# Kernel optimization log

Measured on AMD Instinct MI355X. Metric: run time of the kernel, lower is better.

## Reference

```python
import jax, jax.numpy as jnp
import numpy as np

B, T, E, H = 2, 2048, 1024, 16
S = E // H
LN_EPS = 1e-5


def _layer_norm(x, w, b):
    # normalize over last axis (head dim s)
    mu = jnp.mean(x, axis=-1, keepdims=True)
    var = jnp.mean(jnp.square(x - mu), axis=-1, keepdims=True)
    return (x - mu) * jax.lax.rsqrt(var + LN_EPS) * w + b


def setup_inputs() -> dict:
    key = jax.random.key(0)
    ks = jax.random.split(key, 7)
    scale = 0.02
    return {
        "queries": jax.random.normal(ks[0], (B, T, E), dtype=jnp.float32),
        "keys": jax.random.normal(ks[1], (B, T, E), dtype=jnp.float32),
        "values": jax.random.normal(ks[2], (B, T, E), dtype=jnp.float32),
        "Wq": jax.random.normal(ks[3], (E, E), dtype=jnp.float32) * scale,
        "Wk": jax.random.normal(ks[4], (E, E), dtype=jnp.float32) * scale,
        "Wv": jax.random.normal(ks[5], (E, E), dtype=jnp.float32) * scale,
        "Wo": jax.random.normal(ks[6], (E, E), dtype=jnp.float32) * scale,
        "bo": jnp.zeros((E,), dtype=jnp.float32),
        "q_ln_w": jnp.ones((S,), dtype=jnp.float32),
        "q_ln_b": jnp.zeros((S,), dtype=jnp.float32),
        "k_ln_w": jnp.ones((S,), dtype=jnp.float32),
        "k_ln_b": jnp.zeros((S,), dtype=jnp.float32),
    }


def reference(queries, keys, values, Wq, Wk, Wv, Wo, bo, q_ln_w, q_ln_b, k_ln_w, k_ln_b):
    b, tq, e = queries.shape
    tk = keys.shape[1]
    h, s = H, S

    q = (queries @ Wq).reshape(b, tq, h, s)
    k = (keys @ Wk).reshape(b, tk, h, s)
    v = (values @ Wv).reshape(b, tk, h, s)

    # kqnorm: per-head LayerNorm over s
    q = _layer_norm(q, q_ln_w, q_ln_b)
    k = _layer_norm(k, k_ln_w, k_ln_b)

    # NOTE: original scales q and k each by emb**(-1/4) (NOT head_dim)
    inv4 = jnp.asarray(e, q.dtype) ** -0.25
    q = q * inv4
    k = k * inv4

    dot = jnp.einsum("bqhs,bkhs->bhqk", q, k)  # [b,h,tq,tk]

    # causal mask (mask_diagonal=False -> keep diagonal): mask j > i
    causal = jnp.tril(jnp.ones((tq, tk), dtype=bool))
    dot = jnp.where(causal, dot, jnp.asarray(-jnp.inf, dot.dtype))

    attn = jax.nn.softmax(dot, axis=-1)

    out = jnp.einsum("bhqk,bkhs->bqhs", attn, v).reshape(b, tq, e)
    return out @ Wo + bo
```

## Files before the change

### kernel.cpp

```cpp
#include <hip/hip_runtime.h>

#define Tdim 2048
#define Edim 1024
#define Hdim 16
#define Sdim 64
#define Mdim 4096
#define LN_EPS 1e-5f
#define QKSCALE 0.21233045007200477f

typedef __bf16 bf16x8 __attribute__((ext_vector_type(8)));
typedef float f32x4 __attribute__((ext_vector_type(4)));

__device__ __forceinline__ unsigned short f2bf(float f) {
  union { float f; unsigned int u; } c; c.f = f;
  unsigned int u = c.u;
  return (unsigned short)((u + 0x7FFFu + ((u >> 16) & 1u)) >> 16);
}

__device__ __forceinline__ float exp2fast(float x) {
  float r;
  asm("v_exp_f32 %0, %1" : "=v"(r) : "v"(x));
  return r;
}

__device__ __forceinline__ void gl_lds16(const void* g, void* l) {
  __builtin_amdgcn_global_load_lds(
      (const __attribute__((address_space(1))) void*)g,
      (__attribute__((address_space(3))) void*)l, 16, 0, 0);
}

__device__ __forceinline__ unsigned int pk2bf(unsigned int lo, unsigned int hi) {
  return __builtin_amdgcn_perm(hi, lo, 0x07060302u);
}

__global__ __launch_bounds__(256) void cvt_k(
    const float* __restrict__ X0, const float* __restrict__ X1, const float* __restrict__ X2,
    unsigned short* __restrict__ Y0, unsigned short* __restrict__ Y1,
    unsigned short* __restrict__ Y2) {
  const float* X = blockIdx.z == 0 ? X0 : blockIdx.z == 1 ? X1 : X2;
  unsigned short* Y = blockIdx.z == 0 ? Y0 : blockIdx.z == 1 ? Y1 : Y2;
  size_t i = ((size_t)blockIdx.x * 256 + threadIdx.x) * 8;
  uint4 a = *(const uint4*)&X[i];
  uint4 b = *(const uint4*)&X[i + 4];
  uint4 o;
  o.x = pk2bf(a.x, a.y);
  o.y = pk2bf(a.z, a.w);
  o.z = pk2bf(b.x, b.y);
  o.w = pk2bf(b.z, b.w);
  *(uint4*)&Y[i] = o;
}

__global__ __launch_bounds__(256) void wconv_k(
    const float* __restrict__ W0, const float* __restrict__ W1,
    const float* __restrict__ W2, const float* __restrict__ W3,
    unsigned short* __restrict__ O0, unsigned short* __restrict__ O1,
    unsigned short* __restrict__ O2, unsigned short* __restrict__ O3) {
  const float* W = blockIdx.z == 0 ? W0 : blockIdx.z == 1 ? W1 : blockIdx.z == 2 ? W2 : W3;
  unsigned short* O = blockIdx.z == 0 ? O0 : blockIdx.z == 1 ? O1 : blockIdx.z == 2 ? O2 : O3;
  __shared__ float tile[32][33];
  int n0 = blockIdx.x * 32, k0 = blockIdx.y * 32;
  int tx = threadIdx.x, ty = threadIdx.y;
  for (int yy = ty; yy < 32; yy += 8)
    tile[yy][tx] = W[(size_t)(k0 + yy) * Edim + n0 + tx];
  __syncthreads();
  for (int yy = ty; yy < 32; yy += 8)
    O[(size_t)(n0 + yy) * Edim + k0 + tx] = f2bf(tile[tx][yy]);
}

__global__ __launch_bounds__(256) void qkv_k(
    const unsigned short* __restrict__ Qa, const unsigned short* __restrict__ Ka,
    const unsigned short* __restrict__ Va,
    const unsigned short* __restrict__ Bq, const unsigned short* __restrict__ Bk,
    const unsigned short* __restrict__ Bv,
    const float* __restrict__ qlnw, const float* __restrict__ qlnb,
    const float* __restrict__ klnw, const float* __restrict__ klnb,
    unsigned short* __restrict__ Oq, unsigned short* __restrict__ Ok,
    unsigned short* __restrict__ Ov) {
  __shared__ unsigned short As[2][128 * 64];
  __shared__ unsigned short Bs[2][128 * 64];
  int f = blockIdx.x;
  int L = (f & 7) * 96 + (f >> 3);
  int bx = L & 7, by = (L >> 3) & 31, z = L >> 8;
  const unsigned short* A = z == 0 ? Qa : z == 1 ? Ka : Va;
  const unsigned short* Bt = z == 0 ? Bq : z == 1 ? Bk : Bv;
  const float* lnw = z == 0 ? qlnw : klnw;
  const float* lnb = z == 0 ? qlnb : klnb;
  unsigned short* obf = z == 0 ? Oq : z == 1 ? Ok : Ov;

  int tid = threadIdx.x, lane = tid & 63, w = tid >> 6;
  int wr = w >> 1, wc = w & 1;
  int lg = lane >> 4, l15 = lane & 15;
  int lr = lane >> 3, ls = lane & 7;
  int m0 = by * 128, n0 = bx * 128;

  f32x4 acc[4][4];
#pragma unroll
  for (int i = 0; i < 4; ++i)
#pragma unroll
    for (int j = 0; j < 4; ++j) acc[i][j] = f32x4{0.f, 0.f, 0.f, 0.f};

  auto stage = [&](int buf, int ks) {
    int k0 = ks * 64;
#pragma unroll
    for (int q = 0; q < 4; ++q) {
      int c = w * 4 + q, r = c * 8 + lr;
      gl_lds16(&A[(size_t)(m0 + r) * Edim + k0 + ((ls ^ (r & 7)) * 8)], &As[buf][c * 512]);
    }
#pragma unroll
    for (int q = 0; q < 4; ++q) {
      int c = w * 4 + q, r = c * 8 + lr;
      gl_lds16(&Bt[(size_t)(n0 + r) * Edim + k0 + ((ls ^ (r & 7)) * 8)], &Bs[buf][c * 512]);
    }
  };

  stage(0, 0);
  for (int ks = 0; ks < 16; ++ks) {
    int cur = ks & 1;
    __syncthreads();
    if (ks + 1 < 16) stage(cur ^ 1, ks + 1);
    const unsigned short* pA = (z == 2) ? &Bs[cur][0] : &As[cur][0];
    const unsigned short* pB = (z == 2) ? &As[cur][0] : &Bs[cur][0];
    __builtin_amdgcn_s_setprio(1);
#pragma unroll
    for (int kx = 0; kx < 2; ++kx) {
      bf16x8 a[4], bb[4];
#pragma unroll
      for (int i = 0; i < 4; ++i) {
        int r = wr * 64 + i * 16 + l15;
        a[i] = *(const bf16x8*)&pA[r * 64 + (((kx * 4 + lg) ^ (r & 7)) * 8)];
      }
#pragma unroll
      for (int j = 0; j < 4; ++j) {
        int r = wc * 64 + j * 16 + l15;
        bb[j] = *(const bf16x8*)&pB[r * 64 + (((kx * 4 + lg) ^ (r & 7)) * 8)];
      }
#pragma unroll
      for (int i = 0; i < 4; ++i)
#pragma unroll
        for (int j = 0; j < 4; ++j)
          acc[i][j] = __builtin_amdgcn_mfma_f32_16x16x32_bf16(a[i], bb[j], acc[i][j], 0, 0, 0);
    }
    __builtin_amdgcn_s_setprio(0);
  }

  if (z < 2) {
    int mb = m0 + wr * 64;
    int h = (n0 >> 6) + wc;
#pragma unroll
    for (int i = 0; i < 4; ++i) {
#pragma unroll
      for (int r = 0; r < 4; ++r) {
        float xv[4];
#pragma unroll
        for (int j = 0; j < 4; ++j) xv[j] = acc[i][j][r];
        float sum = xv[0] + xv[1] + xv[2] + xv[3];
        float sq = xv[0] * xv[0] + xv[1] * xv[1] + xv[2] * xv[2] + xv[3] * xv[3];
#pragma unroll
        for (int off = 1; off < 16; off <<= 1) {
          sum += __shfl_xor(sum, off);
          sq += __shfl_xor(sq, off);
        }
        float mean = sum * (1.f / 64.f);
        float var = sq * (1.f / 64.f) - mean * mean;
        float rstd = rsqrtf(var + LN_EPS);
        int m = mb + i * 16 + (lg << 2) + r;
        int bb2 = m >> 11, tt = m & 2047;
        size_t base = ((size_t)(bb2 * Hdim + h) * Tdim + tt) * Sdim;
#pragma unroll
        for (int j = 0; j < 4; ++j) {
          int s = j * 16 + l15;
          float ov = ((xv[j] - mean) * rstd * lnw[s] + lnb[s]) * QKSCALE;
          obf[base + s] = f2bf(ov);
        }
      }
    }
  } else {
#pragma unroll
    for (int i = 0; i < 4; ++i)
#pragma unroll
      for (int r = 0; r < 4; ++r) {
        int hc = n0 + wr * 64 + i * 16 + (lg << 2) + r;
        int h = hc >> 6, s = hc & 63;
#pragma unroll
        for (int j = 0; j < 4; ++j) {
          int tk = m0 + wc * 64 + j * 16 + l15;
          int bb2 = tk >> 11, tt = tk & 2047;
          obf[(((size_t)(bb2 * Hdim + h) * Sdim + s)) * Tdim + tt] = f2bf(acc[i][j][r]);
        }
      }
  }
}

__global__ __launch_bounds__(256) void gemmo_k(
    const unsigned short* __restrict__ A, const unsigned short* __restrict__ Bt,
    const float* __restrict__ bias, float* __restrict__ ofp) {
  __shared__ unsigned short As[2][128 * 64];
  __shared__ unsigned short Bs[2][64 * 64];
  int f = blockIdx.x;
  int L = (f & 7) * 64 + (f >> 3);
  int bx = L & 15, by = L >> 4;
  int tid = threadIdx.x, lane = tid & 63, w = tid >> 6;
  int wr = w >> 1, wc = w & 1;
  int lg = lane >> 4, l15 = lane & 15;
  int lr = lane >> 3, ls = lane & 7;
  int m0 = by * 128, n0 = bx * 64;

  f32x4 acc[4][2];
#pragma unroll
  for (int i = 0; i < 4; ++i)
#pragma unroll
    for (int j = 0; j < 2; ++j) acc[i][j] = f32x4{0.f, 0.f, 0.f, 0.f};

  auto stage = [&](int buf, int ks) {
    int k0 = ks * 64;
#pragma unroll
    for (int q = 0; q < 4; ++q) {
      int c = w * 4 + q, r = c * 8 + lr;
      gl_lds16(&A[(size_t)(m0 + r) * Edim + k0 + ((ls ^ (r & 7)) * 8)], &As[buf][c * 512]);
    }
#pragma unroll
    for (int q = 0; q < 2; ++q) {
      int c = w * 2 + q, r = c * 8 + lr;
      gl_lds16(&Bt[(size_t)(n0 + r) * Edim + k0 + ((ls ^ (r & 7)) * 8)], &Bs[buf][c * 512]);
    }
  };

  stage(0, 0);
  for (int ks = 0; ks < 16; ++ks) {
    int cur = ks & 1;
    __syncthreads();
    if (ks + 1 < 16) stage(cur ^ 1, ks + 1);
    __builtin_amdgcn_s_setprio(1);
#pragma unroll
    for (int kx = 0; kx < 2; ++kx) {
      bf16x8 a[4], bb[2];
#pragma unroll
      for (int i = 0; i < 4; ++i) {
        int r = wr * 64 + i * 16 + l15;
        a[i] = *(const bf16x8*)&As[cur][r * 64 + (((kx * 4 + lg) ^ (r & 7)) * 8)];
      }
#pragma unroll
      for (int j = 0; j < 2; ++j) {
        int r = wc * 32 + j * 16 + l15;
        bb[j] = *(const bf16x8*)&Bs[cur][r * 64 + (((kx * 4 + lg) ^ (r & 7)) * 8)];
      }
#pragma unroll
      for (int i = 0; i < 4; ++i)
#pragma unroll
        for (int j = 0; j < 2; ++j)
          acc[i][j] = __builtin_amdgcn_mfma_f32_16x16x32_bf16(a[i], bb[j], acc[i][j], 0, 0, 0);
    }
    __builtin_amdgcn_s_setprio(0);
  }

  int mb = m0 + wr * 64, nb = n0 + wc * 32;
#pragma unroll
  for (int i = 0; i < 4; ++i)
#pragma unroll
    for (int r = 0; r < 4; ++r) {
      int m = mb + i * 16 + (lg << 2) + r;
#pragma unroll
      for (int j = 0; j < 2; ++j) {
        int n = nb + j * 16 + l15;
        ofp[(size_t)m * Edim + n] = acc[i][j][r] + bias[n];
      }
    }
}

__global__ __launch_bounds__(256) void flash_k(
    const unsigned short* __restrict__ Qn, const unsigned short* __restrict__ Kn,
    const unsigned short* __restrict__ Vb, unsigned short* __restrict__ Ob) {
  __shared__ unsigned short Qs[4096];
  __shared__ unsigned short Ks[2][4096];
  __shared__ unsigned short Vt[2][4096];
  __shared__ unsigned short Ps[4][1024];

  int wid0 = blockIdx.x;
  int idx = wid0 >> 3;
  int bh = (wid0 & 7) * 4 + (idx & 3);
  int qseg = 31 - (idx >> 2);
  int nt = qseg + 1;

  int tid = threadIdx.x, lane = tid & 63, w = tid >> 6;
  int lg = lane >> 4, l15 = lane & 15;
  int lr = lane >> 3, ls = lane & 7;
  const unsigned short* Qg = Qn + ((size_t)bh * Tdim + (size_t)qseg * 64) * Sdim;
  const unsigned short* Kg = Kn + (size_t)bh * Tdim * Sdim;
  const unsigned short* Vg = Vb + (size_t)bh * Sdim * Tdim;
  int b = bh >> 4, h = bh & 15;

  auto stageK = [&](int tt, int kb) {
    const unsigned short* src = Kg + (size_t)tt * 64 * 64;
#pragma unroll
    for (int q = 0; q < 2; ++q) {
      int c = w * 2 + q, r = c * 8 + lr;
      gl_lds16(&src[r * 64 + ((ls ^ (r & 7)) * 8)], &Ks[kb][c * 512]);
    }
  };
  auto stageV = [&](int tt, int vb) {
    const unsigned short* src = Vg + tt * 64;
#pragma unroll
    for (int q = 0; q < 2; ++q) {
      int c = w * 2 + q, r = c * 8 + lr;
      gl_lds16(&src[(size_t)r * Tdim + ((ls ^ (r & 7)) * 8)], &Vt[vb][c * 512]);
    }
  };

#pragma unroll
  for (int q = 0; q < 2; ++q) {
    int c = w * 2 + q, r = c * 8 + lr;
    gl_lds16(&Qg[r * 64 + ((ls ^ (r & 7)) * 8)], &Qs[c * 512]);
  }
  stageK(0, 0);
  stageV(0, 0);

  float mrun = -1e30f;
  float lrun[4] = {0.f, 0.f, 0.f, 0.f};
  f32x4 o[4];
#pragma unroll
  for (int js = 0; js < 4; ++js) o[js] = f32x4{0.f, 0.f, 0.f, 0.f};

  __syncthreads();

  bf16x8 aq[2];
  {
    int rq = w * 16 + l15;
    aq[0] = *(const bf16x8*)&Qs[rq * 64 + ((lg ^ (rq & 7)) * 8)];
    aq[1] = *(const bf16x8*)&Qs[rq * 64 + (((4 + lg) ^ (rq & 7)) * 8)];
  }

  for (int t = 0; t < nt; ++t) {
    int cur = t & 1;
    if (t + 1 < nt) {
      stageK(t + 1, cur ^ 1);
      stageV(t + 1, cur ^ 1);
    }
    f32x4 sf[4];
#pragma unroll
    for (int j = 0; j < 4; ++j) sf[j] = f32x4{0.f, 0.f, 0.f, 0.f};
    const unsigned short* Kc = &Ks[cur][0];
    __builtin_amdgcn_s_setprio(1);
#pragma unroll
    for (int kx = 0; kx < 2; ++kx) {
#pragma unroll
      for (int j = 0; j < 4; ++j) {
        int rk = j * 16 + l15;
        bf16x8 bk = *(const bf16x8*)&Kc[rk * 64 + (((kx * 4 + lg) ^ (rk & 7)) * 8)];
        sf[j] = __builtin_amdgcn_mfma_f32_16x16x32_bf16(aq[kx], bk, sf[j], 0, 0, 0);
      }
    }
    __builtin_amdgcn_s_setprio(0);
    if (t == qseg) {
#pragma unroll
      for (int j = 0; j < 4; ++j)
#pragma unroll
        for (int rr = 0; rr < 4; ++rr)
          if (j * 16 + l15 > w * 16 + (lg << 2) + rr) sf[j][rr] = -1e30f;
    }
    float mx = -3e38f;
#pragma unroll
    for (int j = 0; j < 4; ++j)
#pragma unroll
      for (int rr = 0; rr < 4; ++rr) mx = fmaxf(mx, sf[j][rr]);
#pragma unroll
    for (int off = 1; off < 16; off <<= 1) mx = fmaxf(mx, __shfl_xor(mx, off));
    if (__any(mx > mrun + 8.f)) {
      float mnew = fmaxf(mrun, mx);
      float alpha = exp2fast(mrun - mnew);
      mrun = mnew;
#pragma unroll
      for (int rr = 0; rr < 4; ++rr) lrun[rr] *= alpha;
#pragma unroll
      for (int js = 0; js < 4; ++js) o[js] *= alpha;
    }
    unsigned short* Pw = &Ps[w][0];
#pragma unroll
    for (int j = 0; j < 4; ++j) {
      int og = 2 * j + (l15 >> 3);
#pragma unroll
      for (int rr = 0; rr < 4; ++rr) {
        float p = exp2fast(sf[j][rr] - mrun);
        lrun[rr] += p;
        union { float f; unsigned int u; } cu;
        cu.f = p;
        int qr = (lg << 2) + rr;
        Pw[qr * 64 + ((og ^ (qr & 7)) * 8) + (l15 & 7)] = (unsigned short)(cu.u >> 16);
      }
    }
    const unsigned short* Vc = &Vt[cur][0];
    __builtin_amdgcn_s_setprio(1);
#pragma unroll
    for (int kx = 0; kx < 2; ++kx) {
      bf16x8 ap = *(const bf16x8*)&Pw[l15 * 64 + (((kx * 4 + lg) ^ (l15 & 7)) * 8)];
#pragma unroll
      for (int js = 0; js < 4; ++js) {
        int rv = js * 16 + l15;
        bf16x8 bv = *(const bf16x8*)&Vc[rv * 64 + (((kx * 4 + lg) ^ (rv & 7)) * 8)];
        o[js] = __builtin_amdgcn_mfma_f32_16x16x32_bf16(ap, bv, o[js], 0, 0, 0);
      }
    }
    __builtin_amdgcn_s_setprio(0);
    __syncthreads();
  }

#pragma unroll
  for (int rr = 0; rr < 4; ++rr) {
    float l = lrun[rr];
#pragma unroll
    for (int off = 1; off < 16; off <<= 1) l += __shfl_xor(l, off);
    float inv = 1.f / l;
    int tg = qseg * 64 + w * 16 + (lg << 2) + rr;
    size_t base = ((size_t)b * Tdim + tg) * Edim + h * 64;
#pragma unroll
    for (int js = 0; js < 4; ++js) Ob[base + js * 16 + l15] = f2bf(o[js][rr] * inv);
  }
}

extern "C" void kernel_launch(void* const* d_in, const int* in_sizes, int n_in,
                              void* d_out, int out_size, void* d_ws, size_t ws_size,
                              hipStream_t stream) {
  const float* queries = (const float*)d_in[0];
  const float* keys    = (const float*)d_in[1];
  const float* values  = (const float*)d_in[2];
  const float* Wq = (const float*)d_in[3];
  const float* Wk = (const float*)d_in[4];
  const float* Wv = (const float*)d_in[5];
  const float* Wo = (const float*)d_in[6];
  const float* bo = (const float*)d_in[7];
  const float* qlnw = (const float*)d_in[8];
  const float* qlnb = (const float*)d_in[9];
  const float* klnw = (const float*)d_in[10];
  const float* klnb = (const float*)d_in[11];
  float* out = (float*)d_out;

  unsigned short* Wtq = (unsigned short*)d_ws;
  unsigned short* Wtk = Wtq + 1024 * 1024;
  unsigned short* Wtv = Wtk + 1024 * 1024;
  unsigned short* Wto = Wtv + 1024 * 1024;
  unsigned short* Qn  = Wto + 1024 * 1024;
  unsigned short* Kn  = Qn + (size_t)Mdim * Edim;
  unsigned short* Vb  = Kn + (size_t)Mdim * Edim;
  unsigned short* Qa  = Vb + (size_t)Mdim * Edim;
  unsigned short* Ka  = Qa + (size_t)Mdim * Edim;
  unsigned short* Va  = Ka + (size_t)Mdim * Edim;
  unsigned short* Ob  = Qa;

  cvt_k<<<dim3(2048, 1, 3), 256, 0, stream>>>(queries, keys, values, Qa, Ka, Va);
  wconv_k<<<dim3(32, 32, 4), dim3(32, 8), 0, stream>>>(Wq, Wk, Wv, Wo, Wtq, Wtk, Wtv, Wto);
  qkv_k<<<768, 256, 0, stream>>>(Qa, Ka, Va, Wtq, Wtk, Wtv,
                                 qlnw, qlnb, klnw, klnb, Qn, Kn, Vb);
  flash_k<<<1024, 256, 0, stream>>>(Qn, Kn, Vb, Ob);
  gemmo_k<<<512, 256, 0, stream>>>(Ob, Wto, bo, out);
}
```

Before: 228.5 us.

## Merge prep kernels and switch GEMMs to single-buffered K=32 tiles for occupancy

Fuses the activation bf16 conversion and the weight transpose-convert into one launch to save a kernel launch. The QKV and output-projection GEMMs drop from double-buffered BK=64 LDS tiles to single-buffered BK=32 tiles with a 4-way swizzle, and add launch_bounds(256,4). The smaller LDS footprint aims to fit more blocks per CU, at the cost of losing the load/compute overlap and adding a second barrier each K step.

```diff
diff --git a/kernel.cpp b/kernel.cpp
--- a/kernel.cpp
+++ b/kernel.cpp
@@ -33,41 +33,45 @@
   return __builtin_amdgcn_perm(hi, lo, 0x07060302u);
 }
 
-__global__ __launch_bounds__(256) void cvt_k(
+__global__ __launch_bounds__(256) void prep_k(
     const float* __restrict__ X0, const float* __restrict__ X1, const float* __restrict__ X2,
     unsigned short* __restrict__ Y0, unsigned short* __restrict__ Y1,
-    unsigned short* __restrict__ Y2) {
-  const float* X = blockIdx.z == 0 ? X0 : blockIdx.z == 1 ? X1 : X2;
-  unsigned short* Y = blockIdx.z == 0 ? Y0 : blockIdx.z == 1 ? Y1 : Y2;
-  size_t i = ((size_t)blockIdx.x * 256 + threadIdx.x) * 8;
-  uint4 a = *(const uint4*)&X[i];
-  uint4 b = *(const uint4*)&X[i + 4];
-  uint4 o;
-  o.x = pk2bf(a.x, a.y);
-  o.y = pk2bf(a.z, a.w);
-  o.z = pk2bf(b.x, b.y);
-  o.w = pk2bf(b.z, b.w);
-  *(uint4*)&Y[i] = o;
-}
-
-__global__ __launch_bounds__(256) void wconv_k(
+    unsigned short* __restrict__ Y2,
     const float* __restrict__ W0, const float* __restrict__ W1,
     const float* __restrict__ W2, const float* __restrict__ W3,
     unsigned short* __restrict__ O0, unsigned short* __restrict__ O1,
     unsigned short* __restrict__ O2, unsigned short* __restrict__ O3) {
-  const float* W = blockIdx.z == 0 ? W0 : blockIdx.z == 1 ? W1 : blockIdx.z == 2 ? W2 : W3;
-  unsigned short* O = blockIdx.z == 0 ? O0 : blockIdx.z == 1 ? O1 : blockIdx.z == 2 ? O2 : O3;
-  __shared__ float tile[32][33];
-  int n0 = blockIdx.x * 32, k0 = blockIdx.y * 32;
-  int tx = threadIdx.x, ty = threadIdx.y;
-  for (int yy = ty; yy < 32; yy += 8)
-    tile[yy][tx] = W[(size_t)(k0 + yy) * Edim + n0 + tx];
-  __syncthreads();
-  for (int yy = ty; yy < 32; yy += 8)
-    O[(size_t)(n0 + yy) * Edim + k0 + tx] = f2bf(tile[tx][yy]);
-}
-
-__global__ __launch_bounds__(256) void qkv_k(
+  int bid = blockIdx.x, tid = threadIdx.x;
+  if (bid < 6144) {
+    int zi = bid >> 11, blk = bid & 2047;
+    const float* X = zi == 0 ? X0 : zi == 1 ? X1 : X2;
+    unsigned short* Y = zi == 0 ? Y0 : zi == 1 ? Y1 : Y2;
+    size_t i = ((size_t)blk * 256 + tid) * 8;
+    uint4 a = *(const uint4*)&X[i];
+    uint4 b = *(const uint4*)&X[i + 4];
+    uint4 o;
+    o.x = pk2bf(a.x, a.y);
+    o.y = pk2bf(a.z, a.w);
+    o.z = pk2bf(b.x, b.y);
+    o.w = pk2bf(b.z, b.w);
+    *(uint4*)&Y[i] = o;
+  } else {
+    int wb = bid - 6144;
+    int zi = wb >> 10, tile = wb & 1023;
+    const float* W = zi == 0 ? W0 : zi == 1 ? W1 : zi == 2 ? W2 : W3;
+    unsigned short* O = zi == 0 ? O0 : zi == 1 ? O1 : zi == 2 ? O2 : O3;
+    __shared__ float t[32][33];
+    int n0 = (tile & 31) * 32, k0 = (tile >> 5) * 32;
+    int tx = tid & 31, ty = tid >> 5;
+    for (int yy = ty; yy < 32; yy += 8)
+      t[yy][tx] = W[(size_t)(k0 + yy) * Edim + n0 + tx];
+    __syncthreads();
+    for (int yy = ty; yy < 32; yy += 8)
+      O[(size_t)(n0 + yy) * Edim + k0 + tx] = f2bf(t[tx][yy]);
+  }
+}
+
+__global__ __launch_bounds__(256, 4) void qkv_k(
     const unsigned short* __restrict__ Qa, const unsigned short* __restrict__ Ka,
     const unsigned short* __restrict__ Va,
     const unsigned short* __restrict__ Bq, const unsigned short* __restrict__ Bk,
@@ -76,8 +80,8 @@
     const float* __restrict__ klnw, const float* __restrict__ klnb,
     unsigned short* __restrict__ Oq, unsigned short* __restrict__ Ok,
     unsigned short* __restrict__ Ov) {
-  __shared__ unsigned short As[2][128 * 64];
-  __shared__ unsigned short Bs[2][128 * 64];
+  __shared__ unsigned short As[128 * 32];
+  __shared__ unsigned short Bs[128 * 32];
   int f = blockIdx.x;
   int L = (f & 7) * 96 + (f >> 3);
   int bx = L & 7, by = (L >> 3) & 31, z = L >> 8;
@@ -90,7 +94,7 @@
   int tid = threadIdx.x, lane = tid & 63, w = tid >> 6;
   int wr = w >> 1, wc = w & 1;
   int lg = lane >> 4, l15 = lane & 15;
-  int lr = lane >> 3, ls = lane & 7;
+  int cr = lane >> 2, sl = lane & 3;
   int m0 = by * 128, n0 = bx * 128;
 
   f32x4 acc[4][4];
@@ -99,47 +103,39 @@
 #pragma unroll
     for (int j = 0; j < 4; ++j) acc[i][j] = f32x4{0.f, 0.f, 0.f, 0.f};
 
-  auto stage = [&](int buf, int ks) {
-    int k0 = ks * 64;
-#pragma unroll
-    for (int q = 0; q < 4; ++q) {
-      int c = w * 4 + q, r = c * 8 + lr;
-      gl_lds16(&A[(size_t)(m0 + r) * Edim + k0 + ((ls ^ (r & 7)) * 8)], &As[buf][c * 512]);
-    }
-#pragma unroll
-    for (int q = 0; q < 4; ++q) {
-      int c = w * 4 + q, r = c * 8 + lr;
-      gl_lds16(&Bt[(size_t)(n0 + r) * Edim + k0 + ((ls ^ (r & 7)) * 8)], &Bs[buf][c * 512]);
-    }
-  };
-
-  stage(0, 0);
-  for (int ks = 0; ks < 16; ++ks) {
-    int cur = ks & 1;
-    __syncthreads();
-    if (ks + 1 < 16) stage(cur ^ 1, ks + 1);
-    const unsigned short* pA = (z == 2) ? &Bs[cur][0] : &As[cur][0];
-    const unsigned short* pB = (z == 2) ? &As[cur][0] : &Bs[cur][0];
+  for (int ks = 0; ks < 32; ++ks) {
+    int k0 = ks * 32;
+    __syncthreads();
+#pragma unroll
+    for (int q = 0; q < 2; ++q) {
+      int c = w * 2 + q, r = c * 16 + cr;
+      gl_lds16(&A[(size_t)(m0 + r) * Edim + k0 + ((sl ^ (r & 3)) * 8)], &As[c * 512]);
+    }
+#pragma unroll
+    for (int q = 0; q < 2; ++q) {
+      int c = w * 2 + q, r = c * 16 + cr;
+      gl_lds16(&Bt[(size_t)(n0 + r) * Edim + k0 + ((sl ^ (r & 3)) * 8)], &Bs[c * 512]);
+    }
+    __syncthreads();
+    const unsigned short* pA = (z == 2) ? &Bs[0] : &As[0];
+    const unsigned short* pB = (z == 2) ? &As[0] : &Bs[0];
+    bf16x8 a[4], bb[4];
+#pragma unroll
+    for (int i = 0; i < 4; ++i) {
+      int r = wr * 64 + i * 16 + l15;
+      a[i] = *(const bf16x8*)&pA[r * 32 + ((lg ^ (r & 3)) * 8)];
+    }
+#pragma unroll
+    for (int j = 0; j < 4; ++j) {
+      int r = wc * 64 + j * 16 + l15;
+      bb[j] = *(const bf16x8*)&pB[r * 32 + ((lg ^ (r & 3)) * 8)];
+    }
     __builtin_amdgcn_s_setprio(1);
 #pragma unroll
-    for (int kx = 0; kx < 2; ++kx) {
-      bf16x8 a[4], bb[4];
-#pragma unroll
-      for (int i = 0; i < 4; ++i) {
-        int r = wr * 64 + i * 16 + l15;
-        a[i] = *(const bf16x8*)&pA[r * 64 + (((kx * 4 + lg) ^ (r & 7)) * 8)];
-      }
-#pragma unroll
-      for (int j = 0; j < 4; ++j) {
-        int r = wc * 64 + j * 16 + l15;
-        bb[j] = *(const bf16x8*)&pB[r * 64 + (((kx * 4 + lg) ^ (r & 7)) * 8)];
-      }
-#pragma unroll
-      for (int i = 0; i < 4; ++i)
-#pragma unroll
-        for (int j = 0; j < 4; ++j)
-          acc[i][j] = __builtin_amdgcn_mfma_f32_16x16x32_bf16(a[i], bb[j], acc[i][j], 0, 0, 0);
-    }
+    for (int i = 0; i < 4; ++i)
+#pragma unroll
+      for (int j = 0; j < 4; ++j)
+        acc[i][j] = __builtin_amdgcn_mfma_f32_16x16x32_bf16(a[i], bb[j], acc[i][j], 0, 0, 0);
     __builtin_amdgcn_s_setprio(0);
   }
 
@@ -191,18 +187,18 @@
   }
 }
 
-__global__ __launch_bounds__(256) void gemmo_k(
+__global__ __launch_bounds__(256, 4) void gemmo_k(
     const unsigned short* __restrict__ A, const unsigned short* __restrict__ Bt,
     const float* __restrict__ bias, float* __restrict__ ofp) {
-  __shared__ unsigned short As[2][128 * 64];
-  __shared__ unsigned short Bs[2][64 * 64];
+  __shared__ unsigned short As[128 * 32];
+  __shared__ unsigned short Bs[64 * 32];
   int f = blockIdx.x;
   int L = (f & 7) * 64 + (f >> 3);
   int bx = L & 15, by = L >> 4;
   int tid = threadIdx.x, lane = tid & 63, w = tid >> 6;
   int wr = w >> 1, wc = w & 1;
   int lg = lane >> 4, l15 = lane & 15;
-  int lr = lane >> 3, ls = lane & 7;
+  int cr = lane >> 2, sl = lane & 3;
   int m0 = by * 128, n0 = bx * 64;
 
   f32x4 acc[4][2];
@@ -211,45 +207,36 @@
 #pragma unroll
     for (int j = 0; j < 2; ++j) acc[i][j] = f32x4{0.f, 0.f, 0.f, 0.f};
 
-  auto stage = [&](int buf, int ks) {
-    int k0 = ks * 64;
-#pragma unroll
-    for (int q = 0; q < 4; ++q) {
-      int c = w * 4 + q, r = c * 8 + lr;
-      gl_lds16(&A[(size_t)(m0 + r) * Edim + k0 + ((ls ^ (r & 7)) * 8)], &As[buf][c * 512]);
-    }
+  for (int ks = 0; ks < 32; ++ks) {
+    int k0 = ks * 32;
+    __syncthreads();
 #pragma unroll
     for (int q = 0; q < 2; ++q) {
-      int c = w * 2 + q, r = c * 8 + lr;
-      gl_lds16(&Bt[(size_t)(n0 + r) * Edim + k0 + ((ls ^ (r & 7)) * 8)], &Bs[buf][c * 512]);
-    }
-  };
-
-  stage(0, 0);
-  for (int ks = 0; ks < 16; ++ks) {
-    int cur = ks & 1;
-    __syncthreads();
-    if (ks + 1 < 16) stage(cur ^ 1, ks + 1);
+      int c = w * 2 + q, r = c * 16 + cr;
+      gl_lds16(&A[(size_t)(m0 + r) * Edim + k0 + ((sl ^ (r & 3)) * 8)], &As[c * 512]);
+    }
+    {
+      int c = w, r = c * 16 + cr;
+      gl_lds16(&Bt[(size_t)(n0 + r) * Edim + k0 + ((sl ^ (r & 3)) * 8)], &Bs[c * 512]);
+    }
+    __syncthreads();
+    bf16x8 a[4], bb[2];
+#pragma unroll
+    for (int i = 0; i < 4; ++i) {
+      int r = wr * 64 + i * 16 + l15;
+      a[i] = *(const bf16x8*)&As[r * 32 + ((lg ^ (r & 3)) * 8)];
+    }
+#pragma unroll
+    for (int j = 0; j < 2; ++j) {
+      int r = wc * 32 + j * 16 + l15;
+      bb[j] = *(const bf16x8*)&Bs[r * 32 + ((lg ^ (r & 3)) * 8)];
+    }
     __builtin_amdgcn_s_setprio(1);
 #pragma unroll
-    for (int kx = 0; kx < 2; ++kx) {
-      bf16x8 a[4], bb[2];
-#pragma unroll
-      for (int i = 0; i < 4; ++i) {
-        int r = wr * 64 + i * 16 + l15;
-        a[i] = *(const bf16x8*)&As[cur][r * 64 + (((kx * 4 + lg) ^ (r & 7)) * 8)];
-      }
-#pragma unroll
-      for (int j = 0; j < 2; ++j) {
-        int r = wc * 32 + j * 16 + l15;
-        bb[j] = *(const bf16x8*)&Bs[cur][r * 64 + (((kx * 4 + lg) ^ (r & 7)) * 8)];
-      }
-#pragma unroll
-      for (int i = 0; i < 4; ++i)
-#pragma unroll
-        for (int j = 0; j < 2; ++j)
-          acc[i][j] = __builtin_amdgcn_mfma_f32_16x16x32_bf16(a[i], bb[j], acc[i][j], 0, 0, 0);
-    }
+    for (int i = 0; i < 4; ++i)
+#pragma unroll
+      for (int j = 0; j < 2; ++j)
+        acc[i][j] = __builtin_amdgcn_mfma_f32_16x16x32_bf16(a[i], bb[j], acc[i][j], 0, 0, 0);
     __builtin_amdgcn_s_setprio(0);
   }
 
@@ -445,8 +432,8 @@
   unsigned short* Va  = Ka + (size_t)Mdim * Edim;
   unsigned short* Ob  = Qa;
 
-  cvt_k<<<dim3(2048, 1, 3), 256, 0, stream>>>(queries, keys, values, Qa, Ka, Va);
-  wconv_k<<<dim3(32, 32, 4), dim3(32, 8), 0, stream>>>(Wq, Wk, Wv, Wo, Wtq, Wtk, Wtv, Wto);
+  prep_k<<<10240, 256, 0, stream>>>(queries, keys, values, Qa, Ka, Va,
+                                    Wq, Wk, Wv, Wo, Wtq, Wtk, Wtv, Wto);
   qkv_k<<<768, 256, 0, stream>>>(Qa, Ka, Va, Wtq, Wtk, Wtv,
                                  qlnw, qlnb, klnw, klnb, Qn, Kn, Vb);
   flash_k<<<1024, 256, 0, stream>>>(Qn, Kn, Vb, Ob);
```

Result: faster. 220.7 us (-3.4%).
